# Performance work log

Hardware: AMD Instinct MI355X
Metric: run time of the kernel (lower is better)

The kernel has to match this reference:

```python
import jax, jax.numpy as jnp
import numpy as np

NUM_REGIONS = 3
REGION_SIZE = 384
IMG_SIZE = 512
PEAK_WINDOW = 5


def setup_inputs() -> dict:
    key = jax.random.key(0)
    ks = jax.random.split(key, 6)
    B, C, Hf, Wf = 32, 1024, 32, 32
    features = jax.random.normal(ks[0], (B, C, Hf, Wf), jnp.float32)
    cam_32x32 = jax.random.uniform(ks[1], (B, 32, 32), jnp.float32)
    original = jax.random.normal(ks[2], (B, 3, IMG_SIZE, IMG_SIZE), jnp.float32)
    def init_w(k, o, i):
        return jax.random.normal(k, (o, i), jnp.float32) * (1.0 / np.sqrt(i).astype(np.float32))
    w1 = init_w(ks[3], 512, C); b1 = jnp.zeros((512,), jnp.float32)
    w2 = init_w(ks[4], 256, 512); b2 = jnp.zeros((256,), jnp.float32)
    w3 = init_w(ks[5], 1, 256); b3 = jnp.zeros((1,), jnp.float32)
    return dict(features=features, cam_32x32=cam_32x32, original=original,
                w1=w1, b1=b1, w2=w2, b2=b2, w3=w3, b3=b3)


def _attention(features, w1, b1, w2, b2, w3, b3):
    # stack of 1x1 convs == per-pixel matmuls
    h = jax.nn.relu(jnp.einsum('bchw,oc->bohw', features, w1) + b1[None, :, None, None])
    h = jax.nn.relu(jnp.einsum('bchw,oc->bohw', h, w2) + b2[None, :, None, None])
    return jax.nn.sigmoid(jnp.einsum('bchw,oc->bohw', h, w3) + b3[None, :, None, None])


def _pick_peaks(score_map, K):
    # iterative argmax + square-window suppression (NMS-style peak picking)
    Hf, Wf = score_map.shape
    ys = jnp.arange(Hf)[:, None]
    xs = jnp.arange(Wf)[None, :]
    def step(scores, _):
        flat = jnp.argmax(scores)
        val = scores.reshape(-1)[flat]
        fy = (flat // Wf).astype(jnp.int32)
        fx = (flat % Wf).astype(jnp.int32)
        valid = val > 0.0
        fy = jnp.where(valid, fy, Hf // 2).astype(jnp.int32)
        fx = jnp.where(valid, fx, Wf // 2).astype(jnp.int32)
        supp = (jnp.abs(ys - fy) <= PEAK_WINDOW) & (jnp.abs(xs - fx) <= PEAK_WINDOW)
        return jnp.where(supp, jnp.zeros_like(scores), scores), jnp.stack([fy, fx])
    _, peaks = jax.lax.scan(step, score_map, None, length=K)
    return peaks  # [K, 2] (fy, fx)


def reference(features, cam_32x32, original, w1, b1, w2, b2, w3, b3):
    B, C, Hf, Wf = features.shape
    att = _attention(features, w1, b1, w2, b2, w3, b3)  # [B,1,Hf,Wf]
    # bilinear (align_corners=False) resize of CAM to feature grid
    cam_f = jax.image.resize(cam_32x32[:, None], (B, 1, Hf, Wf), 'bilinear')
    att = (att + cam_f) * 0.5

    peaks = jax.vmap(lambda m: _pick_peaks(m, NUM_REGIONS))(att[:, 0])  # [B,K,2]
    sy = IMG_SIZE / float(Hf)
    sx = IMG_SIZE / float(Wf)
    cy = jnp.floor(peaks[..., 0].astype(jnp.float32) * sy).astype(jnp.int32)
    cx = jnp.floor(peaks[..., 1].astype(jnp.float32) * sx).astype(jnp.int32)
    half = REGION_SIZE // 2
    # clamp-and-adjust logic collapses to a clip when img >= region size
    y1 = jnp.clip(cy - half, 0, IMG_SIZE - REGION_SIZE)
    x1 = jnp.clip(cx - half, 0, IMG_SIZE - REGION_SIZE)

    Cimg = original.shape[1]
    def crop_img(img, y1s, x1s):
        return jax.vmap(lambda y, x: jax.lax.dynamic_slice(
            img, (0, y, x), (Cimg, REGION_SIZE, REGION_SIZE)))(y1s, x1s)
    regions = jax.vmap(crop_img)(original, y1, x1)  # [B,K,3,rs,rs]
    regions = regions.reshape(B * NUM_REGIONS, Cimg, REGION_SIZE, REGION_SIZE)
    coords = jnp.stack([x1, y1, x1 + REGION_SIZE, y1 + REGION_SIZE], axis=-1)  # [B,K,4]
    return regions, coords, att
```

## Files before the change

kernel.cpp:

```cpp
#include <hip/hip_runtime.h>
#include <cstdint>
#include <cmath>


typedef float f4 __attribute__((ext_vector_type(4)));
typedef _Float16 f16x8 __attribute__((ext_vector_type(8)));
typedef int i4 __attribute__((ext_vector_type(4)));

#define M_PIX 32768
#define COORDS_OFF 42467328
#define ATT_OFF 42467712
#define H1LO_OFF 8388608
#define H2_OFF 16777216

#define WH_T 0
#define WL_T 2048
#define FH_T 4096
#define FL_T 6144

__device__ __forceinline__ int swz(int row, int k16) {
    return ((row << 4) + (k16 >> 1)) ^ ((row & 7) << 2);
}

__device__ __forceinline__ int split_pack(float v0, float v1, int& lop) {
    _Float16 h0 = (_Float16)v0, h1 = (_Float16)v1;
    float r0 = v0 - (float)h0, r1 = v1 - (float)h1;
    _Float16 l0 = (_Float16)r0, l1 = (_Float16)r1;
    unsigned int uh0 = __builtin_bit_cast(unsigned short, h0);
    unsigned int uh1 = __builtin_bit_cast(unsigned short, h1);
    unsigned int ul0 = __builtin_bit_cast(unsigned short, l0);
    unsigned int ul1 = __builtin_bit_cast(unsigned short, l1);
    lop = (int)(ul0 | (ul1 << 16));
    return (int)(uh0 | (uh1 << 16));
}

template<int MODE>
__global__ __launch_bounds__(256, 2) void gemm_mfma(
    const float* __restrict__ W, const void* __restrict__ FA,
    const void* __restrict__ FB, const float* __restrict__ bias,
    void* __restrict__ OA, void* __restrict__ OB,
    int Kdim, long fstride, int use_feat)
{
    __shared__ i4 ldsv[2048];
    int* lds = (int*)ldsv;

    const int t = threadIdx.x;
    const int lane = t & 63;
    const int wave = t >> 6;
    const int wn = wave >> 1, wp = wave & 1;
    const int n0  = blockIdx.x * 128;
    const int px0 = blockIdx.y * 128;

    const int rl = t & 127;
    const int kb = (t >> 7) * 16;

    const float* F32 = (const float*)FA;
    const unsigned short* FH16 = (const unsigned short*)FA;
    const unsigned short* FL16 = (const unsigned short*)FB;
    if constexpr (MODE == 0) {
        if (use_feat) F32 += ((size_t)(px0 >> 10) << 20) + (px0 & 1023) + rl;
        else          F32 += px0 + rl;
    } else {
        FH16 += px0 + rl;
        FL16 += px0 + rl;
    }
    const float* Wp = W + (size_t)(n0 + rl) * Kdim + kb;

    f4 acc[4][4];
    #pragma unroll
    for (int i = 0; i < 4; ++i)
        #pragma unroll
        for (int j = 0; j < 4; ++j) acc[i][j] = (f4){0.f, 0.f, 0.f, 0.f};

    float fv[16];
    unsigned short hv[16], lv[16];
    f4 wv[4];

    auto LOADS = [&](int k0) {
        if constexpr (MODE == 0) {
            #pragma unroll
            for (int j = 0; j < 16; ++j)
                fv[j] = F32[(size_t)(k0 + kb + j) * fstride];
        } else {
            #pragma unroll
            for (int j = 0; j < 16; ++j) {
                hv[j] = FH16[(size_t)(k0 + kb + j) * fstride];
                lv[j] = FL16[(size_t)(k0 + kb + j) * fstride];
            }
        }
        #pragma unroll
        for (int g = 0; g < 4; ++g)
            wv[g] = *(const f4*)(Wp + k0 + 4 * g);
    };

    auto STAGE = [&]() {
        #pragma unroll
        for (int g = 0; g < 2; ++g) {
            i4 hp, lp;
            #pragma unroll
            for (int j = 0; j < 4; ++j) {
                const int e = 8 * g + 2 * j;
                int lo;
                hp[j] = split_pack(wv[e >> 2][e & 3], wv[(e + 1) >> 2][(e + 1) & 3], lo);
                lp[j] = lo;
            }
            *(i4*)&lds[WH_T + swz(rl, kb + 8 * g)] = hp;
            *(i4*)&lds[WL_T + swz(rl, kb + 8 * g)] = lp;
        }
        #pragma unroll
        for (int g = 0; g < 2; ++g) {
            i4 hp, lp;
            if constexpr (MODE == 0) {
                #pragma unroll
                for (int j = 0; j < 4; ++j) {
                    int lo;
                    hp[j] = split_pack(fv[8 * g + 2 * j], fv[8 * g + 2 * j + 1], lo);
                    lp[j] = lo;
                }
            } else {
                #pragma unroll
                for (int j = 0; j < 4; ++j) {
                    hp[j] = (int)((unsigned int)hv[8 * g + 2 * j] |
                                  ((unsigned int)hv[8 * g + 2 * j + 1] << 16));
                    lp[j] = (int)((unsigned int)lv[8 * g + 2 * j] |
                                  ((unsigned int)lv[8 * g + 2 * j + 1] << 16));
                }
            }
            *(i4*)&lds[FH_T + swz(rl, kb + 8 * g)] = hp;
            *(i4*)&lds[FL_T + swz(rl, kb + 8 * g)] = lp;
        }
    };

    const int rA0 = 64 * wn + (lane & 15);
    const int rB0 = 64 * wp + (lane & 15);
    const int kg  = (lane >> 4) * 8;

    LOADS(0);
    for (int k0 = 0; k0 < Kdim; k0 += 32) {
        STAGE();
        if (k0 + 32 < Kdim) LOADS(k0 + 32);
        __syncthreads();

        f16x8 bh[4], bl[4];
        #pragma unroll
        for (int nf = 0; nf < 4; ++nf) {
            bh[nf] = *(const f16x8*)&lds[FH_T + swz(rB0 + 16 * nf, kg)];
            bl[nf] = *(const f16x8*)&lds[FL_T + swz(rB0 + 16 * nf, kg)];
        }
        #pragma unroll
        for (int m = 0; m < 4; ++m) {
            f16x8 ah = *(const f16x8*)&lds[WH_T + swz(rA0 + 16 * m, kg)];
            f16x8 al = *(const f16x8*)&lds[WL_T + swz(rA0 + 16 * m, kg)];
            #pragma unroll
            for (int nf = 0; nf < 4; ++nf) {
                acc[m][nf] = __builtin_amdgcn_mfma_f32_16x16x32_f16(ah, bh[nf], acc[m][nf], 0, 0, 0);
                acc[m][nf] = __builtin_amdgcn_mfma_f32_16x16x32_f16(ah, bl[nf], acc[m][nf], 0, 0, 0);
                acc[m][nf] = __builtin_amdgcn_mfma_f32_16x16x32_f16(al, bh[nf], acc[m][nf], 0, 0, 0);
            }
        }
        __syncthreads();
    }

    const int pxE = px0 + 64 * wp + (lane & 15);
    const int nE  = n0 + 64 * wn + 4 * (lane >> 4);
    unsigned short* o16a = (unsigned short*)OA;
    unsigned short* o16b = (unsigned short*)OB;
    float* o32 = (float*)OA;
    #pragma unroll
    for (int m = 0; m < 4; ++m) {
        const int n_m = nE + 16 * m;
        const f4 bv = *(const f4*)&bias[n_m];
        #pragma unroll
        for (int nf = 0; nf < 4; ++nf) {
            const int p = pxE + 16 * nf;
            #pragma unroll
            for (int r = 0; r < 4; ++r) {
                float v = fmaxf(acc[m][nf][r] + bv[r], 0.0f);
                if constexpr (MODE == 0) {
                    _Float16 h = (_Float16)v;
                    _Float16 l = (_Float16)(v - (float)h);
                    o16a[(size_t)(n_m + r) * M_PIX + p] = __builtin_bit_cast(unsigned short, h);
                    o16b[(size_t)(n_m + r) * M_PIX + p] = __builtin_bit_cast(unsigned short, l);
                } else {
                    o32[(size_t)(n_m + r) * M_PIX + p] = v;
                }
            }
        }
    }
}

__global__ __launch_bounds__(256) void layer3_att(
    const float* __restrict__ h2, const float* __restrict__ w3,
    const float* __restrict__ b3, const float* __restrict__ cam,
    float* __restrict__ att)
{
    const int p = blockIdx.x * 256 + threadIdx.x;
    float s = b3[0];
    #pragma unroll 8
    for (int k = 0; k < 256; ++k)
        s = fmaf(w3[k], h2[(size_t)k * M_PIX + p], s);
    const float sg = 1.0f / (1.0f + expf(-s));
    att[p] = (sg + cam[p]) * 0.5f;
}

__global__ __launch_bounds__(64) void peaks_kernel(
    const float* __restrict__ att, float* __restrict__ coords,
    int* __restrict__ wsyx)
{
    const int b = blockIdx.x;
    const int lane = threadIdx.x;
    __shared__ float s[1024];
    for (int i = lane; i < 1024; i += 64) s[i] = att[b * 1024 + i];
    __syncthreads();

    for (int kpk = 0; kpk < 3; ++kpk) {
        float bv = -1.0f;
        int bi = 0x7fffffff;
        for (int i = lane; i < 1024; i += 64) {
            float v = s[i];
            if (v > bv) { bv = v; bi = i; }
        }
        for (int off = 32; off >= 1; off >>= 1) {
            float ov = __shfl_down(bv, off);
            int   oi = __shfl_down(bi, off);
            if (ov > bv || (ov == bv && oi < bi)) { bv = ov; bi = oi; }
        }
        bv = __shfl(bv, 0);
        bi = __shfl(bi, 0);

        int fy, fx;
        if (bv > 0.0f) { fy = bi >> 5; fx = bi & 31; }
        else           { fy = 16;      fx = 16; }

        for (int i = lane; i < 1024; i += 64) {
            const int y = i >> 5, x = i & 31;
            const int dy = y > fy ? y - fy : fy - y;
            const int dx = x > fx ? x - fx : fx - x;
            if (dy <= 5 && dx <= 5) s[i] = 0.0f;
        }
        __syncthreads();

        if (lane == 0) {
            int y1 = fy * 16 - 192; y1 = y1 < 0 ? 0 : (y1 > 128 ? 128 : y1);
            int x1 = fx * 16 - 192; x1 = x1 < 0 ? 0 : (x1 > 128 ? 128 : x1);
            const int idx = b * 3 + kpk;
            coords[idx * 4 + 0] = (float)x1;
            coords[idx * 4 + 1] = (float)y1;
            coords[idx * 4 + 2] = (float)(x1 + 384);
            coords[idx * 4 + 3] = (float)(y1 + 384);
            wsyx[idx * 2 + 0] = y1;
            wsyx[idx * 2 + 1] = x1;
        }
        __syncthreads();
    }
}

__global__ __launch_bounds__(256) void crop_kernel(
    const float* __restrict__ orig, const int* __restrict__ wsyx,
    float* __restrict__ out)
{
    const int id = blockIdx.x * 256 + threadIdx.x;
    const int r    = id / (3 * 384 * 96);
    const int rem  = id - r * (3 * 384 * 96);
    const int c    = rem / (384 * 96);
    const int rem2 = rem - c * (384 * 96);
    const int row  = rem2 / 96;
    const int col  = (rem2 - row * 96) * 4;
    const int b = r / 3;
    const int y1 = wsyx[r * 2], x1 = wsyx[r * 2 + 1];
    const float* src = orig + (size_t)b * 786432 + (size_t)c * 262144
                     + (size_t)(y1 + row) * 512 + x1 + col;
    *(f4*)(out + (size_t)id * 4) = *(const f4*)src;
}

extern "C" void kernel_launch(void* const* d_in, const int* in_sizes, int n_in,
                              void* d_out, int out_size, void* d_ws, size_t ws_size,
                              hipStream_t stream)
{
    const float* features = (const float*)d_in[0];
    const float* cam      = (const float*)d_in[1];
    const float* original = (const float*)d_in[2];
    const float* w1 = (const float*)d_in[3];
    const float* b1 = (const float*)d_in[4];
    const float* w2 = (const float*)d_in[5];
    const float* b2 = (const float*)d_in[6];
    const float* w3 = (const float*)d_in[7];
    const float* b3 = (const float*)d_in[8];

    float* out    = (float*)d_out;
    unsigned short* h1hi = (unsigned short*)out;
    unsigned short* h1lo = (unsigned short*)(out + H1LO_OFF);
    float* h2     = out + H2_OFF;
    float* att    = out + ATT_OFF;
    float* coords = out + COORDS_OFF;
    int*   wsyx   = (int*)d_ws;

    dim3 b256(256);
    gemm_mfma<0><<<dim3(4, 256), b256, 0, stream>>>(
        w1, features, nullptr, b1, h1hi, h1lo, 1024, 1024L, 1);
    gemm_mfma<1><<<dim3(2, 256), b256, 0, stream>>>(
        w2, h1hi, h1lo, b2, h2, nullptr, 512, (long)M_PIX, 0);
    layer3_att<<<dim3(128), b256, 0, stream>>>(h2, w3, b3, cam, att);
    peaks_kernel<<<dim3(32), dim3(64), 0, stream>>>(att, coords, wsyx);
    crop_kernel<<<dim3(41472), b256, 0, stream>>>(original, wsyx, out);
}
```

Measured before the change: 506.5 us.

## Pre-split weights into fp16 hi/lo planes and async-load them to LDS

Adds a split_plane pre-pass that converts W1 and W2 into fp16 hi/lo planes once, stored in scratch space inside the output buffer. The GEMM then loads the weight tiles straight into double-buffered LDS with global_load_lds, in a swizzled order, instead of reading fp32 weights, splitting them in registers and writing them to LDS on every tile. The block index is also remapped so groups of 8 pixel blocks share a weight block, which should improve cache reuse. The cost is two extra kernel launches and more LDS per block (48KB), which could lower occupancy.

```diff
diff --git a/kernel.cpp b/kernel.cpp
--- a/kernel.cpp
+++ b/kernel.cpp
@@ -6,17 +6,25 @@
 typedef float f4 __attribute__((ext_vector_type(4)));
 typedef _Float16 f16x8 __attribute__((ext_vector_type(8)));
 typedef int i4 __attribute__((ext_vector_type(4)));
+typedef unsigned short u16x4 __attribute__((ext_vector_type(4)));
 
 #define M_PIX 32768
 #define COORDS_OFF 42467328
 #define ATT_OFF 42467712
 #define H1LO_OFF 8388608
 #define H2_OFF 16777216
-
-#define WH_T 0
-#define WL_T 2048
-#define FH_T 4096
-#define FL_T 6144
+#define W1HI_OFF 25165824
+#define W1LO_OFF 25427968
+#define W2HI_OFF 25690112
+#define W2LO_OFF 25755648
+
+#define FH_T 8192
+#define FL_T 10240
+
+#define GLOAD16(gp, lp) \
+    __builtin_amdgcn_global_load_lds( \
+        (const __attribute__((address_space(1))) unsigned int*)(gp), \
+        (__attribute__((address_space(3))) unsigned int*)(lp), 16, 0, 0)
 
 __device__ __forceinline__ int swz(int row, int k16) {
     return ((row << 4) + (k16 >> 1)) ^ ((row & 7) << 2);
@@ -34,22 +42,45 @@
     return (int)(uh0 | (uh1 << 16));
 }
 
-template<int MODE>
+__global__ __launch_bounds__(256) void split_plane(
+    const float* __restrict__ src, unsigned short* __restrict__ hi,
+    unsigned short* __restrict__ lo, int n4)
+{
+    const int i = blockIdx.x * 256 + threadIdx.x;
+    if (i >= n4) return;
+    f4 v = *(const f4*)(src + 4 * (size_t)i);
+    u16x4 hv, lv;
+    #pragma unroll
+    for (int j = 0; j < 4; ++j) {
+        _Float16 h = (_Float16)v[j];
+        _Float16 l = (_Float16)(v[j] - (float)h);
+        hv[j] = __builtin_bit_cast(unsigned short, h);
+        lv[j] = __builtin_bit_cast(unsigned short, l);
+    }
+    *(u16x4*)(hi + 4 * (size_t)i) = hv;
+    *(u16x4*)(lo + 4 * (size_t)i) = lv;
+}
+
+template<int MODE, int NBL>
 __global__ __launch_bounds__(256, 2) void gemm_mfma(
-    const float* __restrict__ W, const void* __restrict__ FA,
-    const void* __restrict__ FB, const float* __restrict__ bias,
-    void* __restrict__ OA, void* __restrict__ OB,
+    const unsigned short* __restrict__ WH, const unsigned short* __restrict__ WL,
+    const void* __restrict__ FA, const void* __restrict__ FB,
+    const float* __restrict__ bias, void* __restrict__ OA, void* __restrict__ OB,
     int Kdim, long fstride, int use_feat)
 {
-    __shared__ i4 ldsv[2048];
+    __shared__ i4 ldsv[3072];
     int* lds = (int*)ldsv;
 
     const int t = threadIdx.x;
     const int lane = t & 63;
     const int wave = t >> 6;
     const int wn = wave >> 1, wp = wave & 1;
-    const int n0  = blockIdx.x * 128;
-    const int px0 = blockIdx.y * 128;
+
+    const int f = blockIdx.x;
+    const int nb = (f >> 3) & ((1 << NBL) - 1);
+    const int pb = (f & 7) | ((f >> (3 + NBL)) << 3);
+    const int n0  = nb * 128;
+    const int px0 = pb * 128;
 
     const int rl = t & 127;
     const int kb = (t >> 7) * 16;
@@ -64,7 +95,16 @@
         FH16 += px0 + rl;
         FL16 += px0 + rl;
     }
-    const float* Wp = W + (size_t)(n0 + rl) * Kdim + kb;
+
+    int wg_off[2];
+    #pragma unroll
+    for (int j = 0; j < 2; ++j) {
+        const int i  = 2 * wave + j;
+        const int rL = 16 * i + (lane >> 2);
+        const int r  = (rL & 4) ? (rL ^ 1) : rL;
+        const int c  = (4 * (lane & 3)) ^ ((r & 3) << 2);
+        wg_off[j] = (n0 + r) * Kdim + 2 * c;
+    }
 
     f4 acc[4][4];
     #pragma unroll
@@ -74,9 +114,18 @@
 
     float fv[16];
     unsigned short hv[16], lv[16];
-    f4 wv[4];
-
-    auto LOADS = [&](int k0) {
+
+    auto W_GLOADS = [&](int buf, int k0) {
+        const int wb = buf * 4096;
+        #pragma unroll
+        for (int j = 0; j < 2; ++j) {
+            const int i = 2 * wave + j;
+            GLOAD16(WH + wg_off[j] + k0, &lds[wb + 256 * i]);
+            GLOAD16(WL + wg_off[j] + k0, &lds[wb + 2048 + 256 * i]);
+        }
+    };
+
+    auto LOADS_F = [&](int k0) {
         if constexpr (MODE == 0) {
             #pragma unroll
             for (int j = 0; j < 16; ++j)
@@ -88,25 +137,9 @@
                 lv[j] = FL16[(size_t)(k0 + kb + j) * fstride];
             }
         }
-        #pragma unroll
-        for (int g = 0; g < 4; ++g)
-            wv[g] = *(const f4*)(Wp + k0 + 4 * g);
     };
 
-    auto STAGE = [&]() {
-        #pragma unroll
-        for (int g = 0; g < 2; ++g) {
-            i4 hp, lp;
-            #pragma unroll
-            for (int j = 0; j < 4; ++j) {
-                const int e = 8 * g + 2 * j;
-                int lo;
-                hp[j] = split_pack(wv[e >> 2][e & 3], wv[(e + 1) >> 2][(e + 1) & 3], lo);
-                lp[j] = lo;
-            }
-            *(i4*)&lds[WH_T + swz(rl, kb + 8 * g)] = hp;
-            *(i4*)&lds[WL_T + swz(rl, kb + 8 * g)] = lp;
-        }
+    auto STAGE_F = [&]() {
         #pragma unroll
         for (int g = 0; g < 2; ++g) {
             i4 hp, lp;
@@ -135,12 +168,16 @@
     const int rB0 = 64 * wp + (lane & 15);
     const int kg  = (lane >> 4) * 8;
 
-    LOADS(0);
+    W_GLOADS(0, 0);
+    LOADS_F(0);
+    int cur = 0;
     for (int k0 = 0; k0 < Kdim; k0 += 32) {
-        STAGE();
-        if (k0 + 32 < Kdim) LOADS(k0 + 32);
+        STAGE_F();
         __syncthreads();
 
+        if (k0 + 32 < Kdim) { W_GLOADS(cur ^ 1, k0 + 32); LOADS_F(k0 + 32); }
+
+        const int wb = cur * 4096;
         f16x8 bh[4], bl[4];
         #pragma unroll
         for (int nf = 0; nf < 4; ++nf) {
@@ -149,8 +186,8 @@
         }
         #pragma unroll
         for (int m = 0; m < 4; ++m) {
-            f16x8 ah = *(const f16x8*)&lds[WH_T + swz(rA0 + 16 * m, kg)];
-            f16x8 al = *(const f16x8*)&lds[WL_T + swz(rA0 + 16 * m, kg)];
+            f16x8 ah = *(const f16x8*)&lds[wb + swz(rA0 + 16 * m, kg)];
+            f16x8 al = *(const f16x8*)&lds[wb + 2048 + swz(rA0 + 16 * m, kg)];
             #pragma unroll
             for (int nf = 0; nf < 4; ++nf) {
                 acc[m][nf] = __builtin_amdgcn_mfma_f32_16x16x32_f16(ah, bh[nf], acc[m][nf], 0, 0, 0);
@@ -159,6 +196,7 @@
             }
         }
         __syncthreads();
+        cur ^= 1;
     }
 
     const int pxE = px0 + 64 * wp + (lane & 15);
@@ -291,15 +329,21 @@
     unsigned short* h1hi = (unsigned short*)out;
     unsigned short* h1lo = (unsigned short*)(out + H1LO_OFF);
     float* h2     = out + H2_OFF;
+    unsigned short* w1hi = (unsigned short*)(out + W1HI_OFF);
+    unsigned short* w1lo = (unsigned short*)(out + W1LO_OFF);
+    unsigned short* w2hi = (unsigned short*)(out + W2HI_OFF);
+    unsigned short* w2lo = (unsigned short*)(out + W2LO_OFF);
     float* att    = out + ATT_OFF;
     float* coords = out + COORDS_OFF;
     int*   wsyx   = (int*)d_ws;
 
     dim3 b256(256);
-    gemm_mfma<0><<<dim3(4, 256), b256, 0, stream>>>(
-        w1, features, nullptr, b1, h1hi, h1lo, 1024, 1024L, 1);
-    gemm_mfma<1><<<dim3(2, 256), b256, 0, stream>>>(
-        w2, h1hi, h1lo, b2, h2, nullptr, 512, (long)M_PIX, 0);
+    split_plane<<<dim3(512), b256, 0, stream>>>(w1, w1hi, w1lo, 131072);
+    split_plane<<<dim3(128), b256, 0, stream>>>(w2, w2hi, w2lo, 32768);
+    gemm_mfma<0, 2><<<dim3(1024), b256, 0, stream>>>(
+        w1hi, w1lo, features, nullptr, b1, h1hi, h1lo, 1024, 1024L, 1);
+    gemm_mfma<1, 1><<<dim3(512), b256, 0, stream>>>(
+        w2hi, w2lo, h1hi, h1lo, b2, h2, nullptr, 512, (long)M_PIX, 0);
     layer3_att<<<dim3(128), b256, 0, stream>>>(h2, w3, b3, cam, att);
     peaks_kernel<<<dim3(32), dim3(64), 0, stream>>>(att, coords, wsyx);
     crop_kernel<<<dim3(41472), b256, 0, stream>>>(original, wsyx, out);
```

New measurement: 479.6 us. 5.3% less time.
